# Optimization experiments

Measured on AMD Instinct MI355X. Metric: run time of the kernel, lower is better.

The kernel has to match this reference:

```python
import jax, jax.numpy as jnp
import numpy as np

GAMMA = 0.5  # triplet_loss_gamma
B, N, M = 16, 2048, 2048


def setup_inputs() -> dict:
    key = jax.random.key(0)
    k1, k2, k3 = jax.random.split(key, 3)
    scores = jax.random.normal(k1, (B, N + 1, M + 1), dtype=jnp.float32)
    gt_matches0 = jax.random.randint(k2, (B, N), 0, M + 1, dtype=jnp.int32)
    gt_matches1 = jax.random.randint(k3, (B, M), 0, N + 1, dtype=jnp.int32)
    return {"scores": scores, "gt_matches0": gt_matches0, "gt_matches1": gt_matches1}


def reference(scores, gt_matches0, gt_matches1):
    b, n = gt_matches0.shape
    m = gt_matches1.shape[1]
    # -1 means unmatched -> dustbin index (m for rows, n for cols)
    gt0 = jnp.where(gt_matches0 == -1, m, gt_matches0)  # (b, n), values in [0, m]
    gt1 = jnp.where(gt_matches1 == -1, n, gt_matches1)  # (b, m), values in [0, n]

    # ---- anchor = rows (points in cloud 0) ----
    s_rows = scores[:, :n, :]                                  # (b, n, m+1)
    pos0 = jnp.take_along_axis(s_rows, gt0[:, :, None].astype(jnp.int32), axis=2)  # (b, n, 1)
    # negatives: all m columns except the positive one, in order (== boolean-mask gather)
    jidx = jnp.arange(m, dtype=jnp.int32)[None, None, :]       # (1, 1, m)
    neg_j = jidx + (jidx >= gt0[:, :, None]).astype(jnp.int32)  # skip positive column
    neg0 = jnp.take_along_axis(s_rows, neg_j, axis=2)          # (b, n, m)
    # -log(exp(pos)) - (-log(exp(neg))) == neg - pos
    before_clamp1 = neg0 - pos0                                # (b, n, m)
    gap1 = jnp.maximum(before_clamp1 + GAMMA, 0.0)
    loss_mean1 = jnp.mean(jnp.log(jnp.sum(gap1, axis=2) + 1.0), axis=1)  # (b,)

    # ---- anchor = columns (points in cloud 1) ----
    s_cols = scores[:, :, :m]                                  # (b, n+1, m)
    pos1 = jnp.take_along_axis(s_cols, gt1[:, None, :].astype(jnp.int32), axis=1)  # (b, 1, m)
    iidx = jnp.arange(n, dtype=jnp.int32)[None, :, None]       # (1, n, 1)
    neg_i = iidx + (iidx >= gt1[:, None, :]).astype(jnp.int32)  # skip positive row
    neg1 = jnp.take_along_axis(s_cols, neg_i, axis=1)          # (b, n, m)
    before_clamp2 = neg1 - pos1                                # (b, n, m)
    gap2 = jnp.maximum(before_clamp2 + GAMMA, 0.0)
    loss_mean2 = jnp.mean(jnp.log(jnp.sum(gap2, axis=1) + 1.0), axis=1)  # (b,)

    # variance regularizer over all margins (torch.var default: unbiased, ddof=1)
    margin = jnp.concatenate([before_clamp1, before_clamp2], axis=0)  # (2b, n, m)
    var_loss = jnp.log(jnp.var(margin, ddof=1) + 1.0)
    return (loss_mean1 + loss_mean2) / 2.0 + var_loss
```

## Files before the change

kernel.cpp:

```cpp
#include <hip/hip_runtime.h>
#include <math.h>

#define GAMMA 0.5f

constexpr int B_ = 16;
constexpr int N_ = 2048;
constexpr int M_ = 2048;
constexpr int S_ = 2049;
constexpr long long PLANE = (long long)S_ * S_;

constexpr int Q_      = 8;
constexpr int TILE_W  = 512;
constexpr int NTILE   = 4;
constexpr int RPW     = 16;
constexpr int RPB     = 64;
constexpr int NSTRIPE = 33;

constexpr int NDBL = 32;

__global__ void gather_pos(const float* __restrict__ scores,
                           const int* __restrict__ gt0,
                           const int* __restrict__ gt1,
                           float* __restrict__ pos0,
                           float* __restrict__ pos1,
                           double* __restrict__ D) {
  int idx = blockIdx.x * blockDim.x + threadIdx.x;
  if (idx < NDBL) D[idx] = 0.0;
  const int total = B_ * N_;
  if (idx < total) {
    int b = idx >> 11;
    int i = idx & (N_ - 1);
    int g = gt0[idx];
    if (g == -1) g = M_;
    pos0[idx] = scores[(long long)b * PLANE + (long long)i * S_ + g];
  } else if (idx < 2 * total) {
    int k = idx - total;
    int b = k >> 11;
    int j = k & (M_ - 1);
    int g = gt1[k];
    if (g == -1) g = N_;
    pos1[k] = scores[(long long)b * PLANE + (long long)g * S_ + j];
  }
}

__launch_bounds__(256)
__global__ void margin_main(const float* __restrict__ scores,
                            const float* __restrict__ pos0,
                            const float* __restrict__ pos1,
                            float* __restrict__ rowPart,
                            float* __restrict__ colPart,
                            double* __restrict__ D) {
  const int tile = blockIdx.x;
  const int st   = blockIdx.y;
  const int b    = blockIdx.z;
  const int i0   = st * RPB;
  const int j0   = tile * TILE_W;
  const int tid  = threadIdx.x;
  const int lane = tid & 63;
  const int w    = tid >> 6;

  __shared__ float lp0[RPB];
  __shared__ float ldsC[4][TILE_W];
  __shared__ float ldsM[4][8];

  if (tid < RPB) {
    int i = i0 + tid;
    lp0[tid] = (i < N_) ? pos0[b * N_ + i] : 0.0f;
  }

  float p1[Q_], cC[Q_];
#pragma unroll
  for (int q = 0; q < Q_; ++q) {
    p1[q] = pos1[b * M_ + j0 + 64 * q + lane];
    cC[q] = 0.0f;
  }
  float gs = 0.f, gq = 0.f, gsr = 0.f, gqr = 0.f,
        gsc = 0.f, gqc = 0.f, x0 = 0.f, x1 = 0.f;

  __syncthreads();

  const int ib = i0 + w * RPW;
  int rmax = S_ - ib;
  rmax = rmax < 0 ? 0 : (rmax > RPW ? RPW : rmax);
  const float* rowp = scores + (long long)b * PLANE + (long long)ib * S_ + j0 + lane;
  const bool last_tile = (tile == NTILE - 1);

#pragma unroll 4
  for (int r = 0; r < rmax; ++r) {
    const int i = ib + r;
    const float p0 = lp0[w * RPW + r];
    const bool lastrow = (i == N_);

    float s[Q_];
#pragma unroll
    for (int q = 0; q < Q_; ++q) s[q] = rowp[q * 64];
    float extra = 0.0f;
    if (last_tile && lane == 0) extra = rowp[TILE_W];

    float rC = 0.0f;
#pragma unroll
    for (int q = 0; q < Q_; ++q) {
      const float sv = s[q];
      const float sg = sv + GAMMA;
      rC += fmaxf(sg - p0, 0.0f);
      x0  = fmaf(p0, sv, x0);
      cC[q] += fmaxf(sg - p1[q], 0.0f);
      x1  = fmaf(p1[q], sv, x1);
      gs += sv;
      gq  = fmaf(sv, sv, gq);
      if (lastrow) { gsr += sv; gqr = fmaf(sv, sv, gqr); }
    }
    if (last_tile && lane == 0) {
      rC  += fmaxf(extra + GAMMA - p0, 0.0f);
      x0   = fmaf(p0, extra, x0);
      gs  += extra; gq  = fmaf(extra, extra, gq);
      gsc += extra; gqc = fmaf(extra, extra, gqc);
      if (lastrow) { gsr += extra; gqr = fmaf(extra, extra, gqr); }
    }

#pragma unroll
    for (int off = 32; off; off >>= 1) rC += __shfl_xor(rC, off, 64);
    if (lane == 0 && !lastrow)
      rowPart[((long long)tile * B_ + b) * N_ + i] = rC;
    rowp += S_;
  }

  float m0 = gs, m1 = gq, m2 = gsr, m3 = gqr, m4 = gsc, m5 = gqc, m6 = x0, m7 = x1;
#pragma unroll
  for (int off = 32; off; off >>= 1) {
    m0 += __shfl_xor(m0, off, 64); m1 += __shfl_xor(m1, off, 64);
    m2 += __shfl_xor(m2, off, 64); m3 += __shfl_xor(m3, off, 64);
    m4 += __shfl_xor(m4, off, 64); m5 += __shfl_xor(m5, off, 64);
    m6 += __shfl_xor(m6, off, 64); m7 += __shfl_xor(m7, off, 64);
  }
  if (lane == 0) {
    ldsM[w][0] = m0; ldsM[w][1] = m1; ldsM[w][2] = m2; ldsM[w][3] = m3;
    ldsM[w][4] = m4; ldsM[w][5] = m5; ldsM[w][6] = m6; ldsM[w][7] = m7;
  }
#pragma unroll
  for (int q = 0; q < Q_; ++q) ldsC[w][q * 64 + lane] = cC[q];

  __syncthreads();

  {
    const float c0v = ldsC[0][tid] + ldsC[1][tid] + ldsC[2][tid] + ldsC[3][tid];
    const float c1v = ldsC[0][tid + 256] + ldsC[1][tid + 256] +
                      ldsC[2][tid + 256] + ldsC[3][tid + 256];
    const long long base = ((long long)st * B_ + b) * M_ + j0;
    colPart[base + tid] = c0v;
    colPart[base + tid + 256] = c1v;
  }
  if (tid < 8) {
    double v = (double)ldsM[0][tid] + (double)ldsM[1][tid] +
               (double)ldsM[2][tid] + (double)ldsM[3][tid];
    atomicAdd(&D[tid], v);
  }
}

__global__ void finalize(const float* __restrict__ rowPart,
                         const float* __restrict__ colPart,
                         const float* __restrict__ pos0,
                         const float* __restrict__ pos1,
                         double* __restrict__ D,
                         float* __restrict__ out) {
  const int slice = blockIdx.x;
  const int b     = blockIdx.y;
  const int phase = blockIdx.z;
  const int tid   = threadIdx.x;
  const int lane  = tid & 63;
  const int w     = tid >> 6;
  const int idx   = slice * 256 + tid;

  double aL, aP, aPq;
  if (phase == 0) {
    float r = 0.f;
#pragma unroll
    for (int t = 0; t < NTILE; ++t)
      r += rowPart[((long long)t * B_ + b) * N_ + idx];
    float p = pos0[b * N_ + idx];
    aL = log((double)r + 0.5);
    aP = (double)p; aPq = (double)p * p;
  } else {
    float c = 0.f;
    for (int s = 0; s < NSTRIPE; ++s)
      c += colPart[((long long)s * B_ + b) * M_ + idx];
    float p = pos1[b * M_ + idx];
    aL = log((double)c + 0.5);
    aP = (double)p; aPq = (double)p * p;
  }

#pragma unroll
  for (int off = 32; off; off >>= 1) {
    aL  += __shfl_xor(aL, off, 64);
    aP  += __shfl_xor(aP, off, 64);
    aPq += __shfl_xor(aPq, off, 64);
  }
  __shared__ double red[4][3];
  if (lane == 0) { red[w][0] = aL; red[w][1] = aP; red[w][2] = aPq; }
  __syncthreads();
  if (tid == 0) {
    atomicAdd(&D[8 + b], red[0][0] + red[1][0] + red[2][0] + red[3][0]);
    atomicAdd(&D[24 + 2 * phase], red[0][1] + red[1][1] + red[2][1] + red[3][1]);
    atomicAdd(&D[25 + 2 * phase], red[0][2] + red[1][2] + red[2][2] + red[3][2]);
  }

  __shared__ int lastFlag;
  if (tid == 0) {
    __threadfence();
    int* cnt = (int*)(D + 28);
    int old = __hip_atomic_fetch_add(cnt, 1, __ATOMIC_ACQ_REL,
                                     __HIP_MEMORY_SCOPE_AGENT);
    lastFlag = (old == 8 * B_ * 2 - 1);
  }
  __syncthreads();
  if (lastFlag && tid == 0) {
    double Dv[28];
    for (int k = 0; k < 28; ++k)
      Dv[k] = __hip_atomic_load(&D[k], __ATOMIC_RELAXED,
                                __HIP_MEMORY_SCOPE_AGENT);
    const double G1 = Dv[0], G2 = Dv[1], G1r = Dv[2], G2r = Dv[3];
    const double G1c = Dv[4], G2c = Dv[5], X0 = Dv[6], X1 = Dv[7];
    const double P0 = Dv[24], P0q = Dv[25], P1 = Dv[26], P1q = Dv[27];
    const double SM = 2.0 * G1 - G1r - G1c - 2049.0 * (P0 + P1);
    const double SQ = 2.0 * G2 - G2r - G2c - 2.0 * (X0 + X1)
                      + 2049.0 * (P0q + P1q);
    const double cnt_ = 134217728.0;
    const double var = (SQ - SM * SM / cnt_) / (cnt_ - 1.0);
    const double vl = log(var + 1.0);
    for (int k = 0; k < B_; ++k)
      out[k] = (float)(Dv[8 + k] / 4096.0 + vl);
  }
}

extern "C" void kernel_launch(void* const* d_in, const int* in_sizes, int n_in,
                              void* d_out, int out_size, void* d_ws, size_t ws_size,
                              hipStream_t stream) {
  const float* scores = (const float*)d_in[0];
  const int*   gt0    = (const int*)d_in[1];
  const int*   gt1    = (const int*)d_in[2];
  float*       out    = (float*)d_out;

  double* D      = (double*)d_ws;
  float* pos0    = (float*)((char*)d_ws + 256);
  float* pos1    = pos0 + (size_t)B_ * N_;
  float* rowPart = pos1 + (size_t)B_ * M_;
  float* colPart = rowPart + (size_t)NTILE * B_ * N_;

  const int gth = 2 * B_ * N_;
  gather_pos<<<(gth + 255) / 256, 256, 0, stream>>>(scores, gt0, gt1,
                                                    pos0, pos1, D);

  dim3 grid(NTILE, NSTRIPE, B_);
  margin_main<<<grid, 256, 0, stream>>>(scores, pos0, pos1,
                                        rowPart, colPart, D);

  dim3 fgrid(8, B_, 2);
  finalize<<<fgrid, 256, 0, stream>>>(rowPart, colPart, pos0, pos1, D, out);
}
```

Measured before the change: 83.14 us.

## Fuse positive-score gather into main kernel and atomically accumulate column sums

Removes the separate gather kernel. Each margin block now gathers its own row and column positive scores straight from scores into shared memory, and contributes the pos sums and squared sums to the double accumulators. The 33rd stripe block, which only handled the dustbin row, is folded into the last wave by letting it process 17 rows. Per-stripe column partials are replaced by float atomicAdds into one column buffer, zeroed by a small init kernel, which removes the 33-stripe reduction loop in finalize. In exchange, column gathers are now repeated per stripe (strided, uncoalesced reads) and float atomics make the column sums order-dependent.

```diff
diff --git a/kernel.cpp b/kernel.cpp
--- a/kernel.cpp
+++ b/kernel.cpp
@@ -14,41 +14,21 @@
 constexpr int NTILE   = 4;
 constexpr int RPW     = 16;
 constexpr int RPB     = 64;
-constexpr int NSTRIPE = 33;
-
+constexpr int NSTRIPE = 32;
 constexpr int NDBL = 32;
 
-__global__ void gather_pos(const float* __restrict__ scores,
-                           const int* __restrict__ gt0,
-                           const int* __restrict__ gt1,
-                           float* __restrict__ pos0,
-                           float* __restrict__ pos1,
-                           double* __restrict__ D) {
+__global__ void init_ws(float4* __restrict__ colC4, double* __restrict__ D) {
   int idx = blockIdx.x * blockDim.x + threadIdx.x;
-  if (idx < NDBL) D[idx] = 0.0;
-  const int total = B_ * N_;
-  if (idx < total) {
-    int b = idx >> 11;
-    int i = idx & (N_ - 1);
-    int g = gt0[idx];
-    if (g == -1) g = M_;
-    pos0[idx] = scores[(long long)b * PLANE + (long long)i * S_ + g];
-  } else if (idx < 2 * total) {
-    int k = idx - total;
-    int b = k >> 11;
-    int j = k & (M_ - 1);
-    int g = gt1[k];
-    if (g == -1) g = N_;
-    pos1[k] = scores[(long long)b * PLANE + (long long)g * S_ + j];
-  }
+  colC4[idx] = make_float4(0.f, 0.f, 0.f, 0.f);
+  if (blockIdx.x == 0 && threadIdx.x < NDBL) D[threadIdx.x] = 0.0;
 }
 
 __launch_bounds__(256)
 __global__ void margin_main(const float* __restrict__ scores,
-                            const float* __restrict__ pos0,
-                            const float* __restrict__ pos1,
+                            const int* __restrict__ gt0,
+                            const int* __restrict__ gt1,
                             float* __restrict__ rowPart,
-                            float* __restrict__ colPart,
+                            float* __restrict__ colC,
                             double* __restrict__ D) {
   const int tile = blockIdx.x;
   const int st   = blockIdx.y;
@@ -59,33 +39,50 @@
   const int lane = tid & 63;
   const int w    = tid >> 6;
 
-  __shared__ float lp0[RPB];
+  __shared__ float lp0[RPB + 1];
+  __shared__ float p1s[TILE_W];
   __shared__ float ldsC[4][TILE_W];
-  __shared__ float ldsM[4][8];
-
-  if (tid < RPB) {
+  __shared__ float ldsM[4][12];
+
+  if (tid <= RPB) {
     int i = i0 + tid;
-    lp0[tid] = (i < N_) ? pos0[b * N_ + i] : 0.0f;
-  }
+    float v = 0.f;
+    if (i < N_) {
+      int g = gt0[b * N_ + i];
+      if (g == -1) g = M_;
+      v = scores[(long long)b * PLANE + (long long)i * S_ + g];
+    }
+    lp0[tid] = v;
+  }
+  {
+    int j = j0 + tid;
+    int g = gt1[b * M_ + j];
+    if (g == -1) g = N_;
+    p1s[tid] = scores[(long long)b * PLANE + (long long)g * S_ + j];
+    j += 256;
+    g = gt1[b * M_ + j];
+    if (g == -1) g = N_;
+    p1s[tid + 256] = scores[(long long)b * PLANE + (long long)g * S_ + j];
+  }
+  __syncthreads();
 
   float p1[Q_], cC[Q_];
 #pragma unroll
   for (int q = 0; q < Q_; ++q) {
-    p1[q] = pos1[b * M_ + j0 + 64 * q + lane];
+    p1[q] = p1s[q * 64 + lane];
     cC[q] = 0.0f;
   }
   float gs = 0.f, gq = 0.f, gsr = 0.f, gqr = 0.f,
         gsc = 0.f, gqc = 0.f, x0 = 0.f, x1 = 0.f;
 
-  __syncthreads();
-
   const int ib = i0 + w * RPW;
+  const int cap = (st == NSTRIPE - 1 && w == 3) ? RPW + 1 : RPW;
   int rmax = S_ - ib;
-  rmax = rmax < 0 ? 0 : (rmax > RPW ? RPW : rmax);
+  rmax = rmax < 0 ? 0 : (rmax > cap ? cap : rmax);
   const float* rowp = scores + (long long)b * PLANE + (long long)ib * S_ + j0 + lane;
   const bool last_tile = (tile == NTILE - 1);
 
-#pragma unroll 4
+#pragma unroll 2
   for (int r = 0; r < rmax; ++r) {
     const int i = ib + r;
     const float p0 = lp0[w * RPW + r];
@@ -125,6 +122,14 @@
     rowp += S_;
   }
 
+  const float pv1a = p1s[tid], pv1b = p1s[tid + 256];
+  float m8 = pv1a + pv1b;
+  float m9 = pv1a * pv1a + pv1b * pv1b;
+  float m10 = 0.f, m11 = 0.f;
+  if (w == 0) {
+    int i = i0 + lane;
+    if (i < N_) { float v = lp0[lane]; m10 = v; m11 = v * v; }
+  }
   float m0 = gs, m1 = gq, m2 = gsr, m3 = gqr, m4 = gsc, m5 = gqc, m6 = x0, m7 = x1;
 #pragma unroll
   for (int off = 32; off; off >>= 1) {
@@ -132,10 +137,13 @@
     m2 += __shfl_xor(m2, off, 64); m3 += __shfl_xor(m3, off, 64);
     m4 += __shfl_xor(m4, off, 64); m5 += __shfl_xor(m5, off, 64);
     m6 += __shfl_xor(m6, off, 64); m7 += __shfl_xor(m7, off, 64);
+    m8 += __shfl_xor(m8, off, 64); m9 += __shfl_xor(m9, off, 64);
+    m10 += __shfl_xor(m10, off, 64); m11 += __shfl_xor(m11, off, 64);
   }
   if (lane == 0) {
     ldsM[w][0] = m0; ldsM[w][1] = m1; ldsM[w][2] = m2; ldsM[w][3] = m3;
     ldsM[w][4] = m4; ldsM[w][5] = m5; ldsM[w][6] = m6; ldsM[w][7] = m7;
+    ldsM[w][8] = m8; ldsM[w][9] = m9; ldsM[w][10] = m10; ldsM[w][11] = m11;
   }
 #pragma unroll
   for (int q = 0; q < Q_; ++q) ldsC[w][q * 64 + lane] = cC[q];
@@ -146,21 +154,20 @@
     const float c0v = ldsC[0][tid] + ldsC[1][tid] + ldsC[2][tid] + ldsC[3][tid];
     const float c1v = ldsC[0][tid + 256] + ldsC[1][tid + 256] +
                       ldsC[2][tid + 256] + ldsC[3][tid + 256];
-    const long long base = ((long long)st * B_ + b) * M_ + j0;
-    colPart[base + tid] = c0v;
-    colPart[base + tid + 256] = c1v;
-  }
-  if (tid < 8) {
+    atomicAdd(&colC[b * M_ + j0 + tid], c0v);
+    atomicAdd(&colC[b * M_ + j0 + tid + 256], c1v);
+  }
+  if (tid < 12) {
     double v = (double)ldsM[0][tid] + (double)ldsM[1][tid] +
                (double)ldsM[2][tid] + (double)ldsM[3][tid];
-    atomicAdd(&D[tid], v);
+    if (tid < 8)       atomicAdd(&D[tid], v);
+    else if (tid < 10) { if (st == 0)   atomicAdd(&D[18 + tid], v); }
+    else               { if (tile == 0) atomicAdd(&D[14 + tid], v); }
   }
 }
 
 __global__ void finalize(const float* __restrict__ rowPart,
-                         const float* __restrict__ colPart,
-                         const float* __restrict__ pos0,
-                         const float* __restrict__ pos1,
+                         const float* __restrict__ colC,
                          double* __restrict__ D,
                          float* __restrict__ out) {
   const int slice = blockIdx.x;
@@ -171,38 +178,24 @@
   const int w     = tid >> 6;
   const int idx   = slice * 256 + tid;
 
-  double aL, aP, aPq;
+  double aL;
   if (phase == 0) {
     float r = 0.f;
 #pragma unroll
     for (int t = 0; t < NTILE; ++t)
       r += rowPart[((long long)t * B_ + b) * N_ + idx];
-    float p = pos0[b * N_ + idx];
     aL = log((double)r + 0.5);
-    aP = (double)p; aPq = (double)p * p;
   } else {
-    float c = 0.f;
-    for (int s = 0; s < NSTRIPE; ++s)
-      c += colPart[((long long)s * B_ + b) * M_ + idx];
-    float p = pos1[b * M_ + idx];
-    aL = log((double)c + 0.5);
-    aP = (double)p; aPq = (double)p * p;
-  }
-
-#pragma unroll
-  for (int off = 32; off; off >>= 1) {
-    aL  += __shfl_xor(aL, off, 64);
-    aP  += __shfl_xor(aP, off, 64);
-    aPq += __shfl_xor(aPq, off, 64);
-  }
-  __shared__ double red[4][3];
-  if (lane == 0) { red[w][0] = aL; red[w][1] = aP; red[w][2] = aPq; }
-  __syncthreads();
-  if (tid == 0) {
-    atomicAdd(&D[8 + b], red[0][0] + red[1][0] + red[2][0] + red[3][0]);
-    atomicAdd(&D[24 + 2 * phase], red[0][1] + red[1][1] + red[2][1] + red[3][1]);
-    atomicAdd(&D[25 + 2 * phase], red[0][2] + red[1][2] + red[2][2] + red[3][2]);
-  }
+    aL = log((double)colC[b * M_ + idx] + 0.5);
+  }
+
+#pragma unroll
+  for (int off = 32; off; off >>= 1) aL += __shfl_xor(aL, off, 64);
+  __shared__ double red[4];
+  if (lane == 0) red[w] = aL;
+  __syncthreads();
+  if (tid == 0)
+    atomicAdd(&D[8 + b], red[0] + red[1] + red[2] + red[3]);
 
   __shared__ int lastFlag;
   if (tid == 0) {
@@ -241,19 +234,14 @@
   float*       out    = (float*)d_out;
 
   double* D      = (double*)d_ws;
-  float* pos0    = (float*)((char*)d_ws + 256);
-  float* pos1    = pos0 + (size_t)B_ * N_;
-  float* rowPart = pos1 + (size_t)B_ * M_;
-  float* colPart = rowPart + (size_t)NTILE * B_ * N_;
-
-  const int gth = 2 * B_ * N_;
-  gather_pos<<<(gth + 255) / 256, 256, 0, stream>>>(scores, gt0, gt1,
-                                                    pos0, pos1, D);
+  float*  colC   = (float*)((char*)d_ws + 256);
+  float*  rowPart = colC + (size_t)B_ * M_;
+
+  init_ws<<<128, 256, 0, stream>>>((float4*)colC, D);
 
   dim3 grid(NTILE, NSTRIPE, B_);
-  margin_main<<<grid, 256, 0, stream>>>(scores, pos0, pos1,
-                                        rowPart, colPart, D);
+  margin_main<<<grid, 256, 0, stream>>>(scores, gt0, gt1, rowPart, colC, D);
 
   dim3 fgrid(8, B_, 2);
-  finalize<<<fgrid, 256, 0, stream>>>(rowPart, colPart, pos0, pos1, D, out);
-}
+  finalize<<<fgrid, 256, 0, stream>>>(rowPart, colC, D, out);
+}
```

Measured after the change: 84.51 us. About the same (+1.6%).

## Use full-row blocks with vectorized loads, fused row log-sum and atomic column accumulation

Applied to the files above, without the earlier changes.

Each block of margin_main now covers 16 full rows, with each thread loading 8 contiguous floats through vector loads. The row sums are finished in LDS and folded into the per-batch log accumulator inside the main kernel, so the rowPart buffer is gone. Column partials go straight to a shared buffer through float atomics instead of per-stripe partial arrays, and the pos sums move into gather_pos, which leaves finalize handling only columns. In exchange the kernel issues many global float atomics (129 stripes contend per column), adds a memset launch, and the column sums now depend on atomic ordering.

```diff
diff --git a/kernel.cpp b/kernel.cpp
--- a/kernel.cpp
+++ b/kernel.cpp
@@ -10,57 +10,79 @@
 constexpr long long PLANE = (long long)S_ * S_;
 
 constexpr int Q_      = 8;
-constexpr int TILE_W  = 512;
-constexpr int NTILE   = 4;
-constexpr int RPW     = 16;
-constexpr int RPB     = 64;
-constexpr int NSTRIPE = 33;
+constexpr int RPB     = 16;
+constexpr int NSTRIPE = 129;
 
 constexpr int NDBL = 32;
+
+typedef float f4u __attribute__((ext_vector_type(4), aligned(4)));
+typedef float f4a __attribute__((ext_vector_type(4)));
 
 __global__ void gather_pos(const float* __restrict__ scores,
                            const int* __restrict__ gt0,
                            const int* __restrict__ gt1,
                            float* __restrict__ pos0,
                            float* __restrict__ pos1,
+                           float* __restrict__ colC,
                            double* __restrict__ D) {
-  int idx = blockIdx.x * blockDim.x + threadIdx.x;
-  if (idx < NDBL) D[idx] = 0.0;
+  const int idx  = blockIdx.x * blockDim.x + threadIdx.x;
+  const int tid  = threadIdx.x;
+  const int lane = tid & 63;
+  const int w    = tid >> 6;
   const int total = B_ * N_;
+
+  float v;
   if (idx < total) {
+    colC[idx] = 0.0f;
     int b = idx >> 11;
     int i = idx & (N_ - 1);
     int g = gt0[idx];
     if (g == -1) g = M_;
-    pos0[idx] = scores[(long long)b * PLANE + (long long)i * S_ + g];
-  } else if (idx < 2 * total) {
+    v = scores[(long long)b * PLANE + (long long)i * S_ + g];
+    pos0[idx] = v;
+  } else {
     int k = idx - total;
     int b = k >> 11;
     int j = k & (M_ - 1);
     int g = gt1[k];
     if (g == -1) g = N_;
-    pos1[k] = scores[(long long)b * PLANE + (long long)g * S_ + j];
-  }
-}
-
-__launch_bounds__(256)
+    v = scores[(long long)b * PLANE + (long long)g * S_ + j];
+    pos1[k] = v;
+  }
+
+  float m = v, q = v * v;
+#pragma unroll
+  for (int off = 32; off; off >>= 1) {
+    m += __shfl_xor(m, off, 64);
+    q += __shfl_xor(q, off, 64);
+  }
+  __shared__ float redP[4][2];
+  if (lane == 0) { redP[w][0] = m; redP[w][1] = q; }
+  __syncthreads();
+  if (tid < 2) {
+    const int phase = (blockIdx.x >= 128) ? 1 : 0;
+    double s = (double)redP[0][tid] + (double)redP[1][tid] +
+               (double)redP[2][tid] + (double)redP[3][tid];
+    atomicAdd(&D[24 + 2 * phase + tid], s);
+  }
+}
+
+__launch_bounds__(256, 8)
 __global__ void margin_main(const float* __restrict__ scores,
                             const float* __restrict__ pos0,
                             const float* __restrict__ pos1,
-                            float* __restrict__ rowPart,
-                            float* __restrict__ colPart,
+                            float* __restrict__ colC,
                             double* __restrict__ D) {
-  const int tile = blockIdx.x;
-  const int st   = blockIdx.y;
-  const int b    = blockIdx.z;
+  const int st   = blockIdx.x;
+  const int b    = blockIdx.y;
   const int i0   = st * RPB;
-  const int j0   = tile * TILE_W;
   const int tid  = threadIdx.x;
   const int lane = tid & 63;
   const int w    = tid >> 6;
+  const int jbase = w * 512 + 8 * lane;
 
   __shared__ float lp0[RPB];
-  __shared__ float ldsC[4][TILE_W];
+  __shared__ float ldsR[RPB][4];
   __shared__ float ldsM[4][8];
 
   if (tid < RPB) {
@@ -69,33 +91,37 @@
   }
 
   float p1[Q_], cC[Q_];
-#pragma unroll
-  for (int q = 0; q < Q_; ++q) {
-    p1[q] = pos1[b * M_ + j0 + 64 * q + lane];
-    cC[q] = 0.0f;
-  }
+  {
+    const f4a plo = *(const f4a*)&pos1[b * M_ + jbase];
+    const f4a phi = *(const f4a*)&pos1[b * M_ + jbase + 4];
+    p1[0] = plo[0]; p1[1] = plo[1]; p1[2] = plo[2]; p1[3] = plo[3];
+    p1[4] = phi[0]; p1[5] = phi[1]; p1[6] = phi[2]; p1[7] = phi[3];
+  }
+#pragma unroll
+  for (int q = 0; q < Q_; ++q) cC[q] = 0.0f;
   float gs = 0.f, gq = 0.f, gsr = 0.f, gqr = 0.f,
         gsc = 0.f, gqc = 0.f, x0 = 0.f, x1 = 0.f;
 
   __syncthreads();
 
-  const int ib = i0 + w * RPW;
-  int rmax = S_ - ib;
-  rmax = rmax < 0 ? 0 : (rmax > RPW ? RPW : rmax);
-  const float* rowp = scores + (long long)b * PLANE + (long long)ib * S_ + j0 + lane;
-  const bool last_tile = (tile == NTILE - 1);
-
-#pragma unroll 4
+  int rmax = S_ - i0;
+  rmax = rmax < 0 ? 0 : (rmax > RPB ? RPB : rmax);
+  const float* rowp = scores + (long long)b * PLANE + (long long)i0 * S_ + jbase;
+  const bool exlane = (w == 3) && (lane == 63);
+
+#pragma unroll 2
   for (int r = 0; r < rmax; ++r) {
-    const int i = ib + r;
-    const float p0 = lp0[w * RPW + r];
+    const int i = i0 + r;
+    const float p0 = lp0[r];
     const bool lastrow = (i == N_);
 
+    const f4u v0 = *(const f4u*)(rowp);
+    const f4u v1 = *(const f4u*)(rowp + 4);
     float s[Q_];
-#pragma unroll
-    for (int q = 0; q < Q_; ++q) s[q] = rowp[q * 64];
+    s[0] = v0[0]; s[1] = v0[1]; s[2] = v0[2]; s[3] = v0[3];
+    s[4] = v1[0]; s[5] = v1[1]; s[6] = v1[2]; s[7] = v1[3];
     float extra = 0.0f;
-    if (last_tile && lane == 0) extra = rowp[TILE_W];
+    if (exlane) extra = rowp[8];
 
     float rC = 0.0f;
 #pragma unroll
@@ -110,7 +136,7 @@
       gq  = fmaf(sv, sv, gq);
       if (lastrow) { gsr += sv; gqr = fmaf(sv, sv, gqr); }
     }
-    if (last_tile && lane == 0) {
+    if (exlane) {
       rC  += fmaxf(extra + GAMMA - p0, 0.0f);
       x0   = fmaf(p0, extra, x0);
       gs  += extra; gq  = fmaf(extra, extra, gq);
@@ -120,8 +146,7 @@
 
 #pragma unroll
     for (int off = 32; off; off >>= 1) rC += __shfl_xor(rC, off, 64);
-    if (lane == 0 && !lastrow)
-      rowPart[((long long)tile * B_ + b) * N_ + i] = rC;
+    if (lane == 0 && !lastrow) ldsR[r][w] = rC;
     rowp += S_;
   }
 
@@ -137,19 +162,28 @@
     ldsM[w][0] = m0; ldsM[w][1] = m1; ldsM[w][2] = m2; ldsM[w][3] = m3;
     ldsM[w][4] = m4; ldsM[w][5] = m5; ldsM[w][6] = m6; ldsM[w][7] = m7;
   }
-#pragma unroll
-  for (int q = 0; q < Q_; ++q) ldsC[w][q * 64 + lane] = cC[q];
-
   __syncthreads();
 
   {
-    const float c0v = ldsC[0][tid] + ldsC[1][tid] + ldsC[2][tid] + ldsC[3][tid];
-    const float c1v = ldsC[0][tid + 256] + ldsC[1][tid + 256] +
-                      ldsC[2][tid + 256] + ldsC[3][tid + 256];
-    const long long base = ((long long)st * B_ + b) * M_ + j0;
-    colPart[base + tid] = c0v;
-    colPart[base + tid + 256] = c1v;
-  }
+    double aL = 0.0;
+    if (tid < RPB) {
+      int i = i0 + tid;
+      if (i < N_) {
+        float v = ldsR[tid][0] + ldsR[tid][1] + ldsR[tid][2] + ldsR[tid][3];
+        aL = log((double)v + 0.5);
+      }
+    }
+    if (w == 0) {
+#pragma unroll
+      for (int off = 8; off; off >>= 1) aL += __shfl_xor(aL, off, 64);
+      if (lane == 0) atomicAdd(&D[8 + b], aL);
+    }
+  }
+
+#pragma unroll
+  for (int q = 0; q < Q_; ++q)
+    atomicAdd(&colC[b * M_ + jbase + q], cC[q]);
+
   if (tid < 8) {
     double v = (double)ldsM[0][tid] + (double)ldsM[1][tid] +
                (double)ldsM[2][tid] + (double)ldsM[3][tid];
@@ -157,52 +191,24 @@
   }
 }
 
-__global__ void finalize(const float* __restrict__ rowPart,
-                         const float* __restrict__ colPart,
-                         const float* __restrict__ pos0,
-                         const float* __restrict__ pos1,
-                         double* __restrict__ D,
-                         float* __restrict__ out) {
+__global__ void finalize_cols(const float* __restrict__ colC,
+                              double* __restrict__ D,
+                              float* __restrict__ out) {
   const int slice = blockIdx.x;
   const int b     = blockIdx.y;
-  const int phase = blockIdx.z;
   const int tid   = threadIdx.x;
   const int lane  = tid & 63;
   const int w     = tid >> 6;
   const int idx   = slice * 256 + tid;
 
-  double aL, aP, aPq;
-  if (phase == 0) {
-    float r = 0.f;
-#pragma unroll
-    for (int t = 0; t < NTILE; ++t)
-      r += rowPart[((long long)t * B_ + b) * N_ + idx];
-    float p = pos0[b * N_ + idx];
-    aL = log((double)r + 0.5);
-    aP = (double)p; aPq = (double)p * p;
-  } else {
-    float c = 0.f;
-    for (int s = 0; s < NSTRIPE; ++s)
-      c += colPart[((long long)s * B_ + b) * M_ + idx];
-    float p = pos1[b * M_ + idx];
-    aL = log((double)c + 0.5);
-    aP = (double)p; aPq = (double)p * p;
-  }
-
-#pragma unroll
-  for (int off = 32; off; off >>= 1) {
-    aL  += __shfl_xor(aL, off, 64);
-    aP  += __shfl_xor(aP, off, 64);
-    aPq += __shfl_xor(aPq, off, 64);
-  }
-  __shared__ double red[4][3];
-  if (lane == 0) { red[w][0] = aL; red[w][1] = aP; red[w][2] = aPq; }
-  __syncthreads();
-  if (tid == 0) {
-    atomicAdd(&D[8 + b], red[0][0] + red[1][0] + red[2][0] + red[3][0]);
-    atomicAdd(&D[24 + 2 * phase], red[0][1] + red[1][1] + red[2][1] + red[3][1]);
-    atomicAdd(&D[25 + 2 * phase], red[0][2] + red[1][2] + red[2][2] + red[3][2]);
-  }
+  double aL = log((double)colC[b * M_ + idx] + 0.5);
+#pragma unroll
+  for (int off = 32; off; off >>= 1) aL += __shfl_xor(aL, off, 64);
+  __shared__ double red[4];
+  if (lane == 0) red[w] = aL;
+  __syncthreads();
+  if (tid == 0)
+    atomicAdd(&D[8 + b], red[0] + red[1] + red[2] + red[3]);
 
   __shared__ int lastFlag;
   if (tid == 0) {
@@ -210,7 +216,7 @@
     int* cnt = (int*)(D + 28);
     int old = __hip_atomic_fetch_add(cnt, 1, __ATOMIC_ACQ_REL,
                                      __HIP_MEMORY_SCOPE_AGENT);
-    lastFlag = (old == 8 * B_ * 2 - 1);
+    lastFlag = (old == 8 * B_ - 1);
   }
   __syncthreads();
   if (lastFlag && tid == 0) {
@@ -240,20 +246,18 @@
   const int*   gt1    = (const int*)d_in[2];
   float*       out    = (float*)d_out;
 
-  double* D      = (double*)d_ws;
-  float* pos0    = (float*)((char*)d_ws + 256);
-  float* pos1    = pos0 + (size_t)B_ * N_;
-  float* rowPart = pos1 + (size_t)B_ * M_;
-  float* colPart = rowPart + (size_t)NTILE * B_ * N_;
-
-  const int gth = 2 * B_ * N_;
-  gather_pos<<<(gth + 255) / 256, 256, 0, stream>>>(scores, gt0, gt1,
-                                                    pos0, pos1, D);
-
-  dim3 grid(NTILE, NSTRIPE, B_);
-  margin_main<<<grid, 256, 0, stream>>>(scores, pos0, pos1,
-                                        rowPart, colPart, D);
-
-  dim3 fgrid(8, B_, 2);
-  finalize<<<fgrid, 256, 0, stream>>>(rowPart, colPart, pos0, pos1, D, out);
-}
+  double* D    = (double*)d_ws;
+  float* pos0  = (float*)((char*)d_ws + 256);
+  float* pos1  = pos0 + (size_t)B_ * N_;
+  float* colC  = pos1 + (size_t)B_ * M_;
+
+  hipMemsetAsync(D, 0, 256, stream);
+
+  gather_pos<<<256, 256, 0, stream>>>(scores, gt0, gt1, pos0, pos1, colC, D);
+
+  dim3 grid(NSTRIPE, B_);
+  margin_main<<<grid, 256, 0, stream>>>(scores, pos0, pos1, colC, D);
+
+  dim3 fgrid(8, B_);
+  finalize_cols<<<fgrid, 256, 0, stream>>>(colC, D, out);
+}
```

Result: slower. 219.8 us (+164.3%).
